# Performance work log

Hardware: AMD Instinct MI355X
Metric: run time of the kernel (lower is better)

## Reference

```python
import jax, jax.numpy as jnp
import numpy as np

GELU = lambda v: jax.nn.gelu(v, approximate=False)  # torch nn.GELU default (exact erf)


def _gconv(x, w):
    # grouped conv1d, valid padding; w: (C,1,K), groups=C. lax conv = cross-correlation, same as torch.
    return jax.lax.conv_general_dilated(x, w, (1,), [(0, 0)],
                                        dimension_numbers=('NCH', 'OIH', 'NCH'),
                                        feature_group_count=x.shape[1])


def _conv(x, w, b):
    # dense conv1d, kernel 3, padding=1
    y = jax.lax.conv_general_dilated(x, w, (1,), [(1, 1)],
                                     dimension_numbers=('NCH', 'OIH', 'NCH'))
    return y + b[None, :, None]


def setup_inputs() -> dict:
    key = jax.random.key(0)
    ks = jax.random.split(key, 12)
    B, C, L = 8, 64, 2048
    H, FL, HD, TD, level = 32, 8, 64, 16, 3
    Cs = (1 + level) * C  # 256 channels into the ODE
    n = lambda k, s: (jax.random.normal(k, s) * 0.05).astype(jnp.float32)
    z = lambda s: jnp.zeros(s, jnp.float32)
    return dict(
        x=jax.random.normal(ks[0], (B, C, L), jnp.float32),
        # DyWAN_QR params
        sw1=n(ks[1], (H, C)), sb1=z((H,)),
        sw2=n(ks[2], (H, H)), sb2=z((H,)),
        sw3=n(ks[3], (2 * FL, H)), sb3=z((2 * FL,)),
        # ODE time embed / FiLM params
        tw1=n(ks[4], (TD, 1)), tb1=z((TD,)),
        tw2=n(ks[5], (TD, TD)), tb2=z((TD,)),
        cw=n(ks[6], (2 * HD, TD)), cb=z((2 * HD,)),
        # ODE conv stack params
        k1=n(ks[7], (HD, Cs, 3)), kb1=z((HD,)),
        k2=n(ks[8], (HD, HD, 3)), kb2=z((HD,)),
        k3=n(ks[9], (Cs, HD, 3)), kb3=z((Cs,)),
    )


def reference(x, sw1, sb1, sw2, sb2, sw3, sb3, tw1, tb1, tw2, tb2, cw, cb,
              k1, kb1, k2, kb2, k3, kb3):
    B, C, L = x.shape
    level, FL, T = 3, 8, 5

    def dywan(a):
        # stat_net: adaptive max pool over L -> (B,C) -> Linear -> GELU
        feat = GELU(jnp.max(a, axis=-1) @ sw1.T + sb1)
        raw = GELU(feat @ sw2.T + sb2) @ sw3.T + sb3  # (B, 2*FL)
        lo_raw, hi_raw = raw[:, :FL], raw[:, FL:]
        # QR of an (FL,1) column vector == L2 normalization (up to LAPACK sign)
        lo = lo_raw / jnp.linalg.norm(lo_raw, axis=1, keepdims=True)
        hi = hi_raw / jnp.linalg.norm(hi_raw, axis=1, keepdims=True)
        return lo, hi

    pad = FL - 1
    coeffs = [x]
    approx = x
    for _ in range(level):
        lo, hi = dywan(approx)
        lo_f = jnp.broadcast_to(lo.mean(0)[None, None, :], (C, 1, FL))
        hi_f = jnp.broadcast_to(hi.mean(0)[None, None, :], (C, 1, FL))
        ap = jnp.pad(approx, ((0, 0), (0, 0), (pad // 2, pad - pad // 2)), mode='reflect')
        new_approx = _gconv(ap, lo_f)[..., :L]
        coeffs.append(_gconv(ap, hi_f)[..., :L])
        approx = new_approx
    stacked = jnp.concatenate(coeffs, axis=1)  # (B, (1+level)*C, L)

    def ode_f(t, y):
        te = jnp.reshape(t, (1, 1)).astype(y.dtype)
        te = GELU(te @ tw1.T + tb1) @ tw2.T + tb2          # (1, TD)
        cond = te @ cw.T + cb                               # (1, 2*HD)
        hd = cond.shape[1] // 2
        gamma, beta = cond[:, :hd], cond[:, hd:]
        h = _conv(y, k1, kb1)
        h = (1.0 + gamma[:, :, None]) * h + beta[:, :, None]  # FiLM
        h = GELU(h)
        h = GELU(_conv(h, k2, kb2))
        return _conv(h, k3, kb3)

    # dopri5 tableau, fixed grid over linspace(0, 1, T) (b7 = 0, so 6 stages)
    hs = 1.0 / (T - 1)
    y = stacked
    for i in range(T - 1):
        t0 = i * hs
        s1 = ode_f(t0, y)
        s2 = ode_f(t0 + hs / 5, y + hs * (1 / 5) * s1)
        s3 = ode_f(t0 + 3 * hs / 10, y + hs * (3 / 40 * s1 + 9 / 40 * s2))
        s4 = ode_f(t0 + 4 * hs / 5, y + hs * (44 / 45 * s1 - 56 / 15 * s2 + 32 / 9 * s3))
        s5 = ode_f(t0 + 8 * hs / 9, y + hs * (19372 / 6561 * s1 - 25360 / 2187 * s2
                                              + 64448 / 6561 * s3 - 212 / 729 * s4))
        s6 = ode_f(t0 + hs, y + hs * (9017 / 3168 * s1 - 355 / 33 * s2 + 46732 / 5247 * s3
                                      + 49 / 176 * s4 - 5103 / 18656 * s5))
        y = y + hs * (35 / 384 * s1 + 500 / 1113 * s3 + 125 / 192 * s4
                      - 2187 / 6784 * s5 + 11 / 84 * s6)
    ode_out = y

    yl = ode_out[:, :C, :]
    yh0 = ode_out[:, C:2 * C, :]
    yh1 = ode_out[:, 2 * C:3 * C, :]
    yh2 = ode_out[:, 3 * C:4 * C, :]

    dx = ode_f(jnp.float32(1.0), ode_out)
    inner = jnp.sum(stacked * dx, axis=(1, 2))  # (B,)
    ecloss = jnp.mean(inner ** 2)
    return (yl, yh0, yh1, yh2, ecloss)
```

## Files before the change

kernel.cpp:

```cpp
#include <hip/hip_runtime.h>
#include <math.h>

#define B 8
#define C 64
#define L 2048
#define CS 256
#define BCL  (B*C*L)
#define BCSL (B*CS*L)
#define HS 0.25f

typedef unsigned short u16;
typedef unsigned int   u32;
typedef __attribute__((ext_vector_type(8))) short sh8;
typedef __attribute__((ext_vector_type(4))) float f4;
typedef __attribute__((ext_vector_type(8))) unsigned short us8;
typedef __attribute__((ext_vector_type(4))) unsigned short us4;

__device__ __forceinline__ float gelu(float x) {
    return 0.5f * x * (1.0f + erff(x * 0.70710678118654752440f));
}
__device__ __forceinline__ u16 f2b(float f) {
    u32 u = __float_as_uint(f);
    u32 r = u + 0x7FFFu + ((u >> 16) & 1u);
    return (u16)(r >> 16);
}
__device__ __forceinline__ float b2f(u16 h) {
    return __uint_as_float(((u32)h) << 16);
}

struct ComboB { const u16* p[6]; float c[6]; };

__global__ __launch_bounds__(256) void prep_k(const float* __restrict__ w,
        u16* __restrict__ dst, int IC, int OC) {
    int idx = blockIdx.x * 256 + threadIdx.x;
    int OCG = OC >> 4;
    int j = idx & 7, lane = (idx >> 3) & 63, t = idx >> 9;
    int ocg = t % OCG, c = t / OCG;
    int oc = ocg * 16 + (lane & 15);
    int K = c * 32 + ((lane >> 4) & 3) * 8 + j;
    int kk = K / IC, ic = K % IC;
    dst[idx] = f2b(w[((size_t)oc * IC + ic) * 3 + kk]);
}

__global__ void cond25_k(const float* __restrict__ tw1, const float* __restrict__ tb1,
                         const float* __restrict__ tw2, const float* __restrict__ tb2,
                         const float* __restrict__ cw, const float* __restrict__ cb,
                         float* __restrict__ condall) {
    __shared__ float te1[16], te2[16];
    int tix = blockIdx.x;
    int tid = threadIdx.x;
    double add[6] = {0.0, 0.25/5.0, 3.0*0.25/10.0, 4.0*0.25/5.0, 8.0*0.25/9.0, 0.25};
    float t = (tix == 24) ? 1.0f : (float)((double)(tix / 6) * 0.25 + add[tix % 6]);
    if (tid < 16) te1[tid] = gelu(t * tw1[tid] + tb1[tid]);
    __syncthreads();
    if (tid < 16) {
        float s = tb2[tid];
        for (int k = 0; k < 16; ++k) s += te1[k] * tw2[tid*16+k];
        te2[tid] = s;
    }
    __syncthreads();
    float s = cb[tid];
    for (int j = 0; j < 16; ++j) s += te2[j] * cw[tid*16+j];
    condall[tix*128 + tid] = s;
}

template<int NC, int EPI>
__global__ __launch_bounds__(256) void fused_k(ComboB in,
        const u16* __restrict__ wp1, const float* __restrict__ kb1,
        const u16* __restrict__ wp2, const float* __restrict__ kb2,
        const u16* __restrict__ wp3, const float* __restrict__ kb3,
        const float* __restrict__ condall, int tix,
        u16* __restrict__ outSb,
        float* __restrict__ y, u16* __restrict__ yb,
        const u16* __restrict__ s1b, const u16* __restrict__ s3b,
        const u16* __restrict__ s4b, const u16* __restrict__ s5b,
        float* __restrict__ outp, const float* __restrict__ stacked,
        double* __restrict__ inner)
{
    __shared__ u16 xs1[50][264];
    __shared__ u16 h1t[50][72];
    __shared__ u16 h2t[48][72];
    __shared__ double sred[4];
    const int tid = threadIdx.x;
    const int l0  = blockIdx.x * 32;
    const int b   = blockIdx.y;
    const int g0  = l0 - 3;

    for (int i = tid; i < 12*264; i += 256) xs1[38 + i/264][i%264] = 0;
    if (tid < 144) h1t[48 + tid/72][tid%72] = 0;

    for (int idx = tid; idx < 38*32; idx += 256) {
        int r = idx >> 5, c8 = idx & 31;
        int gl = g0 + r;
        us8 val;
        if (gl >= 0 && gl < L) {
            size_t a = ((size_t)b * L + gl) * 256 + c8 * 8;
            us8 v0 = *(const us8*)(in.p[0] + a);
            if (NC == 1) {
                val = v0;
            } else {
                float f[8];
                #pragma unroll
                for (int j = 0; j < 8; ++j) f[j] = b2f(v0[j]);
                #pragma unroll
                for (int t = 1; t < NC; ++t) {
                    us8 vt = *(const us8*)(in.p[t] + a);
                    #pragma unroll
                    for (int j = 0; j < 8; ++j) f[j] += in.c[t] * b2f(vt[j]);
                }
                #pragma unroll
                for (int j = 0; j < 8; ++j) val[j] = f2b(f[j]);
            }
        } else {
            #pragma unroll
            for (int j = 0; j < 8; ++j) val[j] = 0;
        }
        *(us8*)&xs1[r][c8 * 8] = val;
    }
    __syncthreads();

    const int wave = tid >> 6, lane = tid & 63;
    const int nlo = lane & 15, quad = lane >> 4;

    f4 a1[3];
    a1[0] = f4{0.f,0.f,0.f,0.f}; a1[1] = a1[0]; a1[2] = a1[0];
    {
        const sh8* w1 = (const sh8*)wp1;
        for (int c = 0; c < 24; ++c) {
            int kk = c >> 3, ic0 = (c & 7) << 5;
            sh8 A = w1[(c*4 + wave)*64 + lane];
            #pragma unroll
            for (int nf = 0; nf < 3; ++nf) {
                sh8 Bv = *(const sh8*)&xs1[nf*16 + nlo + kk][ic0 + quad*8];
                a1[nf] = __builtin_amdgcn_mfma_f32_16x16x32_bf16(A, Bv, a1[nf], 0, 0, 0);
            }
        }
    }
    {
        const float* cd = condall + tix*128;
        #pragma unroll
        for (int nf = 0; nf < 3; ++nf) {
            int p = nf*16 + nlo;
            int gp = l0 - 2 + p;
            bool ok = (gp >= 0 && gp < L);
            #pragma unroll
            for (int reg = 0; reg < 4; ++reg) {
                int oc = wave*16 + quad*4 + reg;
                float v = (1.f + cd[oc]) * (a1[nf][reg] + kb1[oc]) + cd[64+oc];
                h1t[p][oc] = ok ? f2b(gelu(v)) : (u16)0;
            }
        }
    }
    __syncthreads();

    f4 a2[3];
    a2[0] = f4{0.f,0.f,0.f,0.f}; a2[1] = a2[0]; a2[2] = a2[0];
    {
        const sh8* w2 = (const sh8*)wp2;
        #pragma unroll
        for (int c = 0; c < 6; ++c) {
            int kk = c >> 1, ic0 = (c & 1) << 5;
            sh8 A = w2[(c*4 + wave)*64 + lane];
            #pragma unroll
            for (int nf = 0; nf < 3; ++nf) {
                sh8 Bv = *(const sh8*)&h1t[nf*16 + nlo + kk][ic0 + quad*8];
                a2[nf] = __builtin_amdgcn_mfma_f32_16x16x32_bf16(A, Bv, a2[nf], 0, 0, 0);
            }
        }
    }
    {
        #pragma unroll
        for (int nf = 0; nf < 3; ++nf) {
            int q = nf*16 + nlo;
            int gq = l0 - 1 + q;
            bool ok = (gq >= 0 && gq < L);
            #pragma unroll
            for (int reg = 0; reg < 4; ++reg) {
                int oc = wave*16 + quad*4 + reg;
                h2t[q][oc] = ok ? f2b(gelu(a2[nf][reg] + kb2[oc])) : (u16)0;
            }
        }
    }
    __syncthreads();

    f4 a3[4][2];
    #pragma unroll
    for (int mf = 0; mf < 4; ++mf) {
        a3[mf][0] = f4{0.f,0.f,0.f,0.f}; a3[mf][1] = a3[mf][0];
    }
    {
        const sh8* w3 = (const sh8*)wp3;
        #pragma unroll
        for (int c = 0; c < 6; ++c) {
            int kk = c >> 1, ic0 = (c & 1) << 5;
            sh8 B0 = *(const sh8*)&h2t[nlo + kk][ic0 + quad*8];
            sh8 B1 = *(const sh8*)&h2t[16 + nlo + kk][ic0 + quad*8];
            #pragma unroll
            for (int mf = 0; mf < 4; ++mf) {
                sh8 A = w3[(c*16 + wave*4 + mf)*64 + lane];
                a3[mf][0] = __builtin_amdgcn_mfma_f32_16x16x32_bf16(A, B0, a3[mf][0], 0, 0, 0);
                a3[mf][1] = __builtin_amdgcn_mfma_f32_16x16x32_bf16(A, B1, a3[mf][1], 0, 0, 0);
            }
        }
    }

    if (EPI == 3) {
        double acc = 0.0;
        #pragma unroll
        for (int mf = 0; mf < 4; ++mf)
            #pragma unroll
            for (int nf = 0; nf < 2; ++nf)
                #pragma unroll
                for (int reg = 0; reg < 4; ++reg) {
                    int oc = (wave*4 + mf)*16 + quad*4 + reg;
                    int pos = l0 + nf*16 + nlo;
                    size_t idx = ((size_t)b*CS + oc)*L + pos;
                    float dx = a3[mf][nf][reg] + kb3[oc];
                    acc += (double)stacked[idx] * (double)dx;
                }
        #pragma unroll
        for (int off = 32; off > 0; off >>= 1) acc += __shfl_down(acc, off, 64);
        if (lane == 0) sred[wave] = acc;
        __syncthreads();
        if (tid == 0) atomicAdd(&inner[b], sred[0] + sred[1] + sred[2] + sred[3]);
    } else if (EPI == 0) {
        #pragma unroll
        for (int mf = 0; mf < 4; ++mf) {
            int baseoc = (wave*4 + mf)*16 + quad*4;
            #pragma unroll
            for (int nf = 0; nf < 2; ++nf) {
                int pos = l0 + nf*16 + nlo;
                us4 pk;
                #pragma unroll
                for (int reg = 0; reg < 4; ++reg)
                    pk[reg] = f2b(a3[mf][nf][reg] + kb3[baseoc + reg]);
                *(us4*)(outSb + ((size_t)b*L + pos)*256 + baseoc) = pk;
            }
        }
    } else {
        const float c1 = HS*(35.f/384.f), c3 = HS*(500.f/1113.f),
                    c4 = HS*(125.f/192.f), c5 = -HS*(2187.f/6784.f),
                    c6 = HS*(11.f/84.f);
        #pragma unroll
        for (int mf = 0; mf < 4; ++mf) {
            int baseoc = (wave*4 + mf)*16 + quad*4;
            #pragma unroll
            for (int nf = 0; nf < 2; ++nf) {
                int pos = l0 + nf*16 + nlo;
                size_t ta = ((size_t)b*L + pos)*256 + baseoc;
                us4 v1 = *(const us4*)(s1b + ta);
                us4 v3 = *(const us4*)(s3b + ta);
                us4 v4 = *(const us4*)(s4b + ta);
                us4 v5 = *(const us4*)(s5b + ta);
                us4 pk;
                #pragma unroll
                for (int reg = 0; reg < 4; ++reg) {
                    int oc = baseoc + reg;
                    size_t idx = ((size_t)b*CS + oc)*L + pos;
                    float s6 = a3[mf][nf][reg] + kb3[oc];
                    float yv = y[idx] + c1*b2f(v1[reg]) + c3*b2f(v3[reg])
                             + c4*b2f(v4[reg]) + c5*b2f(v5[reg]) + c6*s6;
                    pk[reg] = f2b(yv);
                    if (EPI == 1) y[idx] = yv;
                    if (EPI == 2) {
                        size_t oidx = (((size_t)(oc >> 6)*B + b)*64 + (oc & 63))*L + pos;
                        outp[oidx] = yv;
                    }
                }
                *(us4*)(yb + ta) = pk;
            }
        }
    }
}

__global__ __launch_bounds__(256) void rowmax_k(const float* __restrict__ a, float* __restrict__ bm) {
    __shared__ float red[256];
    int row = blockIdx.x;
    const float* p = a + (size_t)row * L;
    float m = -1e30f;
    for (int t = threadIdx.x; t < L; t += 256) m = fmaxf(m, p[t]);
    red[threadIdx.x] = m;
    __syncthreads();
    for (int s = 128; s > 0; s >>= 1) {
        if (threadIdx.x < s) red[threadIdx.x] = fmaxf(red[threadIdx.x], red[threadIdx.x + s]);
        __syncthreads();
    }
    if (threadIdx.x == 0) bm[row] = red[0];
}

__global__ __launch_bounds__(256) void mlp_k(const float* __restrict__ bm,
    const float* __restrict__ sw1, const float* __restrict__ sb1,
    const float* __restrict__ sw2, const float* __restrict__ sb2,
    const float* __restrict__ sw3, const float* __restrict__ sb3,
    float* __restrict__ filt) {
    __shared__ float m[8][64], f1[8][32], f2[8][32], raw[8][16], nrm[8][2];
    int tid = threadIdx.x;
    for (int i = tid; i < 512; i += 256) m[i >> 6][i & 63] = bm[i];
    __syncthreads();
    {
        int b = tid >> 5, h = tid & 31;
        float s = sb1[h];
        for (int c = 0; c < 64; ++c) s += m[b][c] * sw1[h*64+c];
        f1[b][h] = gelu(s);
    }
    __syncthreads();
    {
        int b = tid >> 5, h = tid & 31;
        float s = sb2[h];
        for (int k = 0; k < 32; ++k) s += f1[b][k] * sw2[h*32+k];
        f2[b][h] = gelu(s);
    }
    __syncthreads();
    if (tid < 128) {
        int b = tid >> 4, j = tid & 15;
        float s = sb3[j];
        for (int k = 0; k < 32; ++k) s += f2[b][k] * sw3[j*32+k];
        raw[b][j] = s;
    }
    __syncthreads();
    if (tid < 16) {
        int b = tid >> 1, half = tid & 1;
        float s = 0.f;
        for (int j = 0; j < 8; ++j) { float v = raw[b][half*8+j]; s += v*v; }
        nrm[b][half] = sqrtf(s);
    }
    __syncthreads();
    if (tid < 16) {
        int half = tid >> 3;
        float s = 0.f;
        for (int b = 0; b < 8; ++b) s += raw[b][tid] / nrm[b][half];
        filt[tid] = s * 0.125f;
    }
}

__global__ __launch_bounds__(256) void wconv_k(const float* __restrict__ ap,
    const float* __restrict__ filt, float* __restrict__ apOut,
    float* __restrict__ stacked, int lev) {
    __shared__ float f[16];
    if (threadIdx.x < 16) f[threadIdx.x] = filt[threadIdx.x];
    __syncthreads();
    size_t idx = (size_t)blockIdx.x * 256 + threadIdx.x;
    int l = (int)(idx & 2047);
    size_t bc = idx >> 11;
    int c = (int)(bc & 63), b = (int)(bc >> 6);
    const float* row = ap + (bc << 11);
    float lo = 0.f, hi = 0.f;
    #pragma unroll
    for (int k = 0; k < 8; ++k) {
        int mI = l + k - 3;
        mI = mI < 0 ? -mI : (mI >= L ? 2*L - 2 - mI : mI);
        float v = row[mI];
        lo += v * f[k];
        hi += v * f[8+k];
    }
    apOut[idx] = lo;
    stacked[((size_t)b * CS + (size_t)(lev+1) * 64 + c) * L + l] = hi;
}

__global__ __launch_bounds__(256) void copyx_k(const float* __restrict__ x, float* __restrict__ st) {
    size_t i = (size_t)blockIdx.x * 256 + threadIdx.x;
    size_t b = i >> 17, rem = i & 131071;
    st[b * ((size_t)CS*L) + rem] = x[i];
}

__global__ __launch_bounds__(256) void copy4_k(const float* __restrict__ s, float* __restrict__ d) {
    size_t i = (size_t)blockIdx.x * 256 + threadIdx.x;
    ((float4*)d)[i] = ((const float4*)s)[i];
}

__global__ __launch_bounds__(256) void tinit_k(const float* __restrict__ st, u16* __restrict__ yb) {
    __shared__ float t[64][65];
    const int tid = threadIdx.x;
    const int l0 = blockIdx.x * 64, c0 = blockIdx.y * 64, b = blockIdx.z;
    #pragma unroll
    for (int k = 0; k < 16; ++k) {
        int c = k * 4 + (tid >> 6), l = tid & 63;
        t[c][l] = st[((size_t)b*CS + c0 + c) * L + l0 + l];
    }
    __syncthreads();
    #pragma unroll
    for (int k = 0; k < 16; ++k) {
        int p = k * 4 + (tid >> 6), ch = tid & 63;
        yb[((size_t)b * L + l0 + p) * 256 + c0 + ch] = f2b(t[ch][p]);
    }
}

__global__ void ecfin_k(const double* __restrict__ inner, float* __restrict__ out) {
    double s = 0.0;
    for (int b = 0; b < 8; ++b) s += inner[b] * inner[b];
    out[BCSL] = (float)(s / 8.0);
}

extern "C" void kernel_launch(void* const* d_in, const int* in_sizes, int n_in,
                              void* d_out, int out_size, void* d_ws, size_t ws_size,
                              hipStream_t stream) {
    const float* x   = (const float*)d_in[0];
    const float* sw1 = (const float*)d_in[1];
    const float* sb1 = (const float*)d_in[2];
    const float* sw2 = (const float*)d_in[3];
    const float* sb2 = (const float*)d_in[4];
    const float* sw3 = (const float*)d_in[5];
    const float* sb3 = (const float*)d_in[6];
    const float* tw1 = (const float*)d_in[7];
    const float* tb1 = (const float*)d_in[8];
    const float* tw2 = (const float*)d_in[9];
    const float* tb2 = (const float*)d_in[10];
    const float* cw  = (const float*)d_in[11];
    const float* cb  = (const float*)d_in[12];
    const float* k1  = (const float*)d_in[13];
    const float* kb1 = (const float*)d_in[14];
    const float* k2  = (const float*)d_in[15];
    const float* kb2 = (const float*)d_in[16];
    const float* k3  = (const float*)d_in[17];
    const float* kb3 = (const float*)d_in[18];
    float* out = (float*)d_out;

    char* cur = (char*)d_ws;
    auto alloc = [&](size_t bytes) { void* p = cur; cur += (bytes + 255) & ~(size_t)255; return p; };
    float* stacked = (float*)alloc(BCSL * 4);
    float* y       = (float*)alloc(BCSL * 4);
    u16*   yb      = (u16*)  alloc(BCSL * 2);
    u16*   sb[5];
    for (int i = 0; i < 5; ++i) sb[i] = (u16*)alloc(BCSL * 2);
    float* cond  = (float*)alloc(3200 * 4);
    float* bmax  = (float*)alloc(512 * 4);
    float* filt  = (float*)alloc(16 * 4);
    double* inner = (double*)alloc(8 * 8);
    u16* wp1 = (u16*)alloc(49152 * 2);
    u16* wp2 = (u16*)alloc(12288 * 2);
    u16* wp3 = (u16*)alloc(49152 * 2);

    u16 *s1b = sb[0], *s2b = sb[1], *s3b = sb[2], *s4b = sb[3], *s5b = sb[4];

    hipMemsetAsync(inner, 0, 8 * sizeof(double), stream);

    prep_k<<<192, 256, 0, stream>>>(k1, wp1, CS, C);
    prep_k<<<48,  256, 0, stream>>>(k2, wp2, C,  C);
    prep_k<<<192, 256, 0, stream>>>(k3, wp3, C,  CS);
    cond25_k<<<25, 128, 0, stream>>>(tw1, tb1, tw2, tb2, cw, cb, cond);

    copyx_k<<<4096, 256, 0, stream>>>(x, stacked);
    const float* apIn = x;
    float* apBuf[2] = {(float*)s1b, (float*)s2b};
    for (int lev = 0; lev < 3; ++lev) {
        rowmax_k<<<512, 256, 0, stream>>>(apIn, bmax);
        mlp_k<<<1, 256, 0, stream>>>(bmax, sw1, sb1, sw2, sb2, sw3, sb3, filt);
        float* apOut = apBuf[lev & 1];
        wconv_k<<<4096, 256, 0, stream>>>(apIn, filt, apOut, stacked, lev);
        apIn = apOut;
    }
    copy4_k<<<4096, 256, 0, stream>>>(stacked, y);
    tinit_k<<<dim3(32, 4, 8), 256, 0, stream>>>(stacked, yb);

    const float hs = HS;
    dim3 cg(64, 8);
    #define LAUNCH(NC, EPI, CIN, TIX, OUTSB, OUTP, STK) \
        fused_k<NC, EPI><<<cg, 256, 0, stream>>>(CIN, wp1, kb1, wp2, kb2, wp3, kb3, \
            cond, TIX, OUTSB, y, yb, s1b, s3b, s4b, s5b, OUTP, STK, inner)

    for (int i = 0; i < 4; ++i) {
        ComboB cA{}; cA.p[0] = yb;
        LAUNCH(1, 0, cA, i*6+0, s1b, nullptr, nullptr);

        ComboB cB{}; cB.p[0] = yb; cB.p[1] = s1b; cB.c[1] = hs*(1.f/5.f);
        LAUNCH(2, 0, cB, i*6+1, s2b, nullptr, nullptr);

        ComboB cC{}; cC.p[0] = yb;
        cC.p[1] = s1b; cC.c[1] = hs*(3.f/40.f);
        cC.p[2] = s2b; cC.c[2] = hs*(9.f/40.f);
        LAUNCH(3, 0, cC, i*6+2, s3b, nullptr, nullptr);

        ComboB cD{}; cD.p[0] = yb;
        cD.p[1] = s1b; cD.c[1] = hs*(44.f/45.f);
        cD.p[2] = s2b; cD.c[2] = -hs*(56.f/15.f);
        cD.p[3] = s3b; cD.c[3] = hs*(32.f/9.f);
        LAUNCH(4, 0, cD, i*6+3, s4b, nullptr, nullptr);

        ComboB cE{}; cE.p[0] = yb;
        cE.p[1] = s1b; cE.c[1] = hs*(19372.f/6561.f);
        cE.p[2] = s2b; cE.c[2] = -hs*(25360.f/2187.f);
        cE.p[3] = s3b; cE.c[3] = hs*(64448.f/6561.f);
        cE.p[4] = s4b; cE.c[4] = -hs*(212.f/729.f);
        LAUNCH(5, 0, cE, i*6+4, s5b, nullptr, nullptr);

        ComboB cF{}; cF.p[0] = yb;
        cF.p[1] = s1b; cF.c[1] = hs*(9017.f/3168.f);
        cF.p[2] = s2b; cF.c[2] = -hs*(355.f/33.f);
        cF.p[3] = s3b; cF.c[3] = hs*(46732.f/5247.f);
        cF.p[4] = s4b; cF.c[4] = hs*(49.f/176.f);
        cF.p[5] = s5b; cF.c[5] = -hs*(5103.f/18656.f);
        if (i < 3) {
            LAUNCH(6, 1, cF, i*6+5, nullptr, nullptr, nullptr);
        } else {
            LAUNCH(6, 2, cF, i*6+5, nullptr, out, nullptr);
        }
    }

    ComboB cZ{}; cZ.p[0] = yb;
    LAUNCH(1, 3, cZ, 24, nullptr, nullptr, stacked);
    ecfin_k<<<1, 1, 0, stream>>>(inner, out);
    #undef LAUNCH
}
```

Baseline: 775.5 us.

## Halve L-tile, fuse y-update partial sum into stage-6 input load, merge y copy

The fused conv kernel now tiles 16 positions per block instead of 32, doubling the grid to 128x8. This cuts wasted halo MFMA work (48 of 32 padded rows becomes 32 of 16) and lowers shared-memory use, at the cost of proportionally more halo reloads. In the final stage, the RK5 weighted sum of s1,s3,s4,s5 is built while the stage inputs are loaded and kept in shared memory as bf16, which removes a second global read of four stage buffers. The separate y copy kernel is folded into the transpose init kernel, but the extra bf16 rounding of the partial sum adds error.

```diff
diff --git a/kernel.cpp b/kernel.cpp
--- a/kernel.cpp
+++ b/kernel.cpp
@@ -72,24 +72,27 @@
         const float* __restrict__ condall, int tix,
         u16* __restrict__ outSb,
         float* __restrict__ y, u16* __restrict__ yb,
-        const u16* __restrict__ s1b, const u16* __restrict__ s3b,
-        const u16* __restrict__ s4b, const u16* __restrict__ s5b,
         float* __restrict__ outp, const float* __restrict__ stacked,
         double* __restrict__ inner)
 {
-    __shared__ u16 xs1[50][264];
-    __shared__ u16 h1t[50][72];
-    __shared__ u16 h2t[48][72];
+    __shared__ u16 xs1[34][264];
+    __shared__ u16 h1t[34][72];
+    __shared__ u16 h2t[18][72];
+    __shared__ u16 ypart[16][264];
     __shared__ double sred[4];
     const int tid = threadIdx.x;
-    const int l0  = blockIdx.x * 32;
+    const int l0  = blockIdx.x * 16;
     const int b   = blockIdx.y;
     const int g0  = l0 - 3;
 
-    for (int i = tid; i < 12*264; i += 256) xs1[38 + i/264][i%264] = 0;
-    if (tid < 144) h1t[48 + tid/72][tid%72] = 0;
-
-    for (int idx = tid; idx < 38*32; idx += 256) {
+    const float cy1 = HS*(35.f/384.f), cy3 = HS*(500.f/1113.f),
+                cy4 = HS*(125.f/192.f), cy5 = -HS*(2187.f/6784.f),
+                cy6 = HS*(11.f/84.f);
+
+    for (int i = tid; i < 12*264; i += 256) xs1[22 + i/264][i%264] = 0;
+    if (tid < 144) h1t[32 + tid/72][tid%72] = 0;
+
+    for (int idx = tid; idx < 22*32; idx += 256) {
         int r = idx >> 5, c8 = idx & 31;
         int gl = g0 + r;
         us8 val;
@@ -100,16 +103,30 @@
                 val = v0;
             } else {
                 float f[8];
+                float yp[8];
                 #pragma unroll
-                for (int j = 0; j < 8; ++j) f[j] = b2f(v0[j]);
+                for (int j = 0; j < 8; ++j) { f[j] = b2f(v0[j]); yp[j] = 0.f; }
                 #pragma unroll
                 for (int t = 1; t < NC; ++t) {
                     us8 vt = *(const us8*)(in.p[t] + a);
                     #pragma unroll
-                    for (int j = 0; j < 8; ++j) f[j] += in.c[t] * b2f(vt[j]);
+                    for (int j = 0; j < 8; ++j) {
+                        float bv = b2f(vt[j]);
+                        f[j] += in.c[t] * bv;
+                        if ((EPI == 1 || EPI == 2) && (t == 1 || t == 3 || t == 4 || t == 5)) {
+                            float cy = (t == 1) ? cy1 : (t == 3) ? cy3 : (t == 4) ? cy4 : cy5;
+                            yp[j] += cy * bv;
+                        }
+                    }
                 }
                 #pragma unroll
                 for (int j = 0; j < 8; ++j) val[j] = f2b(f[j]);
+                if ((EPI == 1 || EPI == 2) && r >= 3 && r < 19) {
+                    us8 ypk;
+                    #pragma unroll
+                    for (int j = 0; j < 8; ++j) ypk[j] = f2b(yp[j]);
+                    *(us8*)&ypart[r - 3][c8 * 8] = ypk;
+                }
             }
         } else {
             #pragma unroll
@@ -122,15 +139,15 @@
     const int wave = tid >> 6, lane = tid & 63;
     const int nlo = lane & 15, quad = lane >> 4;
 
-    f4 a1[3];
-    a1[0] = f4{0.f,0.f,0.f,0.f}; a1[1] = a1[0]; a1[2] = a1[0];
+    f4 a1[2];
+    a1[0] = f4{0.f,0.f,0.f,0.f}; a1[1] = a1[0];
     {
         const sh8* w1 = (const sh8*)wp1;
         for (int c = 0; c < 24; ++c) {
             int kk = c >> 3, ic0 = (c & 7) << 5;
             sh8 A = w1[(c*4 + wave)*64 + lane];
             #pragma unroll
-            for (int nf = 0; nf < 3; ++nf) {
+            for (int nf = 0; nf < 2; ++nf) {
                 sh8 Bv = *(const sh8*)&xs1[nf*16 + nlo + kk][ic0 + quad*8];
                 a1[nf] = __builtin_amdgcn_mfma_f32_16x16x32_bf16(A, Bv, a1[nf], 0, 0, 0);
             }
@@ -139,10 +156,10 @@
     {
         const float* cd = condall + tix*128;
         #pragma unroll
-        for (int nf = 0; nf < 3; ++nf) {
+        for (int nf = 0; nf < 2; ++nf) {
             int p = nf*16 + nlo;
             int gp = l0 - 2 + p;
-            bool ok = (gp >= 0 && gp < L);
+            bool ok = (p < 20) && (gp >= 0) && (gp < L);
             #pragma unroll
             for (int reg = 0; reg < 4; ++reg) {
                 int oc = wave*16 + quad*4 + reg;
@@ -153,8 +170,8 @@
     }
     __syncthreads();
 
-    f4 a2[3];
-    a2[0] = f4{0.f,0.f,0.f,0.f}; a2[1] = a2[0]; a2[2] = a2[0];
+    f4 a2[2];
+    a2[0] = f4{0.f,0.f,0.f,0.f}; a2[1] = a2[0];
     {
         const sh8* w2 = (const sh8*)wp2;
         #pragma unroll
@@ -162,7 +179,7 @@
             int kk = c >> 1, ic0 = (c & 1) << 5;
             sh8 A = w2[(c*4 + wave)*64 + lane];
             #pragma unroll
-            for (int nf = 0; nf < 3; ++nf) {
+            for (int nf = 0; nf < 2; ++nf) {
                 sh8 Bv = *(const sh8*)&h1t[nf*16 + nlo + kk][ic0 + quad*8];
                 a2[nf] = __builtin_amdgcn_mfma_f32_16x16x32_bf16(A, Bv, a2[nf], 0, 0, 0);
             }
@@ -170,54 +187,50 @@
     }
     {
         #pragma unroll
-        for (int nf = 0; nf < 3; ++nf) {
+        for (int nf = 0; nf < 2; ++nf) {
             int q = nf*16 + nlo;
-            int gq = l0 - 1 + q;
-            bool ok = (gq >= 0 && gq < L);
-            #pragma unroll
-            for (int reg = 0; reg < 4; ++reg) {
-                int oc = wave*16 + quad*4 + reg;
-                h2t[q][oc] = ok ? f2b(gelu(a2[nf][reg] + kb2[oc])) : (u16)0;
-            }
-        }
-    }
-    __syncthreads();
-
-    f4 a3[4][2];
+            if (q < 18) {
+                int gq = l0 - 1 + q;
+                bool ok = (gq >= 0) && (gq < L);
+                #pragma unroll
+                for (int reg = 0; reg < 4; ++reg) {
+                    int oc = wave*16 + quad*4 + reg;
+                    h2t[q][oc] = ok ? f2b(gelu(a2[nf][reg] + kb2[oc])) : (u16)0;
+                }
+            }
+        }
+    }
+    __syncthreads();
+
+    f4 a3[4];
     #pragma unroll
-    for (int mf = 0; mf < 4; ++mf) {
-        a3[mf][0] = f4{0.f,0.f,0.f,0.f}; a3[mf][1] = a3[mf][0];
-    }
+    for (int mf = 0; mf < 4; ++mf) a3[mf] = f4{0.f,0.f,0.f,0.f};
     {
         const sh8* w3 = (const sh8*)wp3;
         #pragma unroll
         for (int c = 0; c < 6; ++c) {
             int kk = c >> 1, ic0 = (c & 1) << 5;
             sh8 B0 = *(const sh8*)&h2t[nlo + kk][ic0 + quad*8];
-            sh8 B1 = *(const sh8*)&h2t[16 + nlo + kk][ic0 + quad*8];
             #pragma unroll
             for (int mf = 0; mf < 4; ++mf) {
                 sh8 A = w3[(c*16 + wave*4 + mf)*64 + lane];
-                a3[mf][0] = __builtin_amdgcn_mfma_f32_16x16x32_bf16(A, B0, a3[mf][0], 0, 0, 0);
-                a3[mf][1] = __builtin_amdgcn_mfma_f32_16x16x32_bf16(A, B1, a3[mf][1], 0, 0, 0);
-            }
-        }
-    }
-
+                a3[mf] = __builtin_amdgcn_mfma_f32_16x16x32_bf16(A, B0, a3[mf], 0, 0, 0);
+            }
+        }
+    }
+
+    const int pos = l0 + nlo;
     if (EPI == 3) {
         double acc = 0.0;
         #pragma unroll
         for (int mf = 0; mf < 4; ++mf)
             #pragma unroll
-            for (int nf = 0; nf < 2; ++nf)
-                #pragma unroll
-                for (int reg = 0; reg < 4; ++reg) {
-                    int oc = (wave*4 + mf)*16 + quad*4 + reg;
-                    int pos = l0 + nf*16 + nlo;
-                    size_t idx = ((size_t)b*CS + oc)*L + pos;
-                    float dx = a3[mf][nf][reg] + kb3[oc];
-                    acc += (double)stacked[idx] * (double)dx;
-                }
+            for (int reg = 0; reg < 4; ++reg) {
+                int oc = (wave*4 + mf)*16 + quad*4 + reg;
+                size_t idx = ((size_t)b*CS + oc)*L + pos;
+                float dx = a3[mf][reg] + kb3[oc];
+                acc += (double)stacked[idx] * (double)dx;
+            }
         #pragma unroll
         for (int off = 32; off > 0; off >>= 1) acc += __shfl_down(acc, off, 64);
         if (lane == 0) sred[wave] = acc;
@@ -227,48 +240,32 @@
         #pragma unroll
         for (int mf = 0; mf < 4; ++mf) {
             int baseoc = (wave*4 + mf)*16 + quad*4;
-            #pragma unroll
-            for (int nf = 0; nf < 2; ++nf) {
-                int pos = l0 + nf*16 + nlo;
-                us4 pk;
-                #pragma unroll
-                for (int reg = 0; reg < 4; ++reg)
-                    pk[reg] = f2b(a3[mf][nf][reg] + kb3[baseoc + reg]);
-                *(us4*)(outSb + ((size_t)b*L + pos)*256 + baseoc) = pk;
-            }
+            us4 pk;
+            #pragma unroll
+            for (int reg = 0; reg < 4; ++reg)
+                pk[reg] = f2b(a3[mf][reg] + kb3[baseoc + reg]);
+            *(us4*)(outSb + ((size_t)b*L + pos)*256 + baseoc) = pk;
         }
     } else {
-        const float c1 = HS*(35.f/384.f), c3 = HS*(500.f/1113.f),
-                    c4 = HS*(125.f/192.f), c5 = -HS*(2187.f/6784.f),
-                    c6 = HS*(11.f/84.f);
         #pragma unroll
         for (int mf = 0; mf < 4; ++mf) {
             int baseoc = (wave*4 + mf)*16 + quad*4;
-            #pragma unroll
-            for (int nf = 0; nf < 2; ++nf) {
-                int pos = l0 + nf*16 + nlo;
-                size_t ta = ((size_t)b*L + pos)*256 + baseoc;
-                us4 v1 = *(const us4*)(s1b + ta);
-                us4 v3 = *(const us4*)(s3b + ta);
-                us4 v4 = *(const us4*)(s4b + ta);
-                us4 v5 = *(const us4*)(s5b + ta);
-                us4 pk;
-                #pragma unroll
-                for (int reg = 0; reg < 4; ++reg) {
-                    int oc = baseoc + reg;
-                    size_t idx = ((size_t)b*CS + oc)*L + pos;
-                    float s6 = a3[mf][nf][reg] + kb3[oc];
-                    float yv = y[idx] + c1*b2f(v1[reg]) + c3*b2f(v3[reg])
-                             + c4*b2f(v4[reg]) + c5*b2f(v5[reg]) + c6*s6;
-                    pk[reg] = f2b(yv);
-                    if (EPI == 1) y[idx] = yv;
-                    if (EPI == 2) {
-                        size_t oidx = (((size_t)(oc >> 6)*B + b)*64 + (oc & 63))*L + pos;
-                        outp[oidx] = yv;
-                    }
+            us4 yp4 = *(const us4*)&ypart[nlo][baseoc];
+            us4 pk;
+            #pragma unroll
+            for (int reg = 0; reg < 4; ++reg) {
+                int oc = baseoc + reg;
+                size_t idx = ((size_t)b*CS + oc)*L + pos;
+                float s6 = a3[mf][reg] + kb3[oc];
+                float yv = y[idx] + b2f(yp4[reg]) + cy6 * s6;
+                pk[reg] = f2b(yv);
+                if (EPI == 1) y[idx] = yv;
+                if (EPI == 2) {
+                    size_t oidx = (((size_t)(oc >> 6)*B + b)*64 + (oc & 63))*L + pos;
+                    outp[oidx] = yv;
                 }
-                *(us4*)(yb + ta) = pk;
-            }
+            }
+            *(us4*)(yb + ((size_t)b*L + pos)*256 + baseoc) = pk;
         }
     }
 }
@@ -363,19 +360,18 @@
     st[b * ((size_t)CS*L) + rem] = x[i];
 }
 
-__global__ __launch_bounds__(256) void copy4_k(const float* __restrict__ s, float* __restrict__ d) {
-    size_t i = (size_t)blockIdx.x * 256 + threadIdx.x;
-    ((float4*)d)[i] = ((const float4*)s)[i];
-}
-
-__global__ __launch_bounds__(256) void tinit_k(const float* __restrict__ st, u16* __restrict__ yb) {
+__global__ __launch_bounds__(256) void tinit_k(const float* __restrict__ st,
+        float* __restrict__ y, u16* __restrict__ yb) {
     __shared__ float t[64][65];
     const int tid = threadIdx.x;
     const int l0 = blockIdx.x * 64, c0 = blockIdx.y * 64, b = blockIdx.z;
     #pragma unroll
     for (int k = 0; k < 16; ++k) {
         int c = k * 4 + (tid >> 6), l = tid & 63;
-        t[c][l] = st[((size_t)b*CS + c0 + c) * L + l0 + l];
+        size_t idx = ((size_t)b*CS + c0 + c) * L + l0 + l;
+        float v = st[idx];
+        y[idx] = v;
+        t[c][l] = v;
     }
     __syncthreads();
     #pragma unroll
@@ -420,8 +416,8 @@
     float* stacked = (float*)alloc(BCSL * 4);
     float* y       = (float*)alloc(BCSL * 4);
     u16*   yb      = (u16*)  alloc(BCSL * 2);
-    u16*   sb[5];
-    for (int i = 0; i < 5; ++i) sb[i] = (u16*)alloc(BCSL * 2);
+    u16*   sbuf[5];
+    for (int i = 0; i < 5; ++i) sbuf[i] = (u16*)alloc(BCSL * 2);
     float* cond  = (float*)alloc(3200 * 4);
     float* bmax  = (float*)alloc(512 * 4);
     float* filt  = (float*)alloc(16 * 4);
@@ -430,7 +426,7 @@
     u16* wp2 = (u16*)alloc(12288 * 2);
     u16* wp3 = (u16*)alloc(49152 * 2);
 
-    u16 *s1b = sb[0], *s2b = sb[1], *s3b = sb[2], *s4b = sb[3], *s5b = sb[4];
+    u16 *s1b = sbuf[0], *s2b = sbuf[1], *s3b = sbuf[2], *s4b = sbuf[3], *s5b = sbuf[4];
 
     hipMemsetAsync(inner, 0, 8 * sizeof(double), stream);
 
@@ -449,14 +445,13 @@
         wconv_k<<<4096, 256, 0, stream>>>(apIn, filt, apOut, stacked, lev);
         apIn = apOut;
     }
-    copy4_k<<<4096, 256, 0, stream>>>(stacked, y);
-    tinit_k<<<dim3(32, 4, 8), 256, 0, stream>>>(stacked, yb);
+    tinit_k<<<dim3(32, 4, 8), 256, 0, stream>>>(stacked, y, yb);
 
     const float hs = HS;
-    dim3 cg(64, 8);
+    dim3 cg(128, 8);
     #define LAUNCH(NC, EPI, CIN, TIX, OUTSB, OUTP, STK) \
         fused_k<NC, EPI><<<cg, 256, 0, stream>>>(CIN, wp1, kb1, wp2, kb2, wp3, kb3, \
-            cond, TIX, OUTSB, y, yb, s1b, s3b, s4b, s5b, OUTP, STK, inner)
+            cond, TIX, OUTSB, y, yb, OUTP, STK, inner)
 
     for (int i = 0; i < 4; ++i) {
         ComboB cA{}; cA.p[0] = yb;
```

Measured after the change: 712.0 us. 1.09x faster.
